# Performance work log

Hardware: AMD Instinct MI355X
Metric: run time of the kernel (lower is better)

The kernel has to match this reference:

```python
import jax, jax.numpy as jnp
import numpy as np


def setup_inputs() -> dict:
    key = jax.random.key(0)
    k1, k2, k3, k4 = jax.random.split(key, 4)
    B, C, N, T = 16, 64, 2048, 24
    x = jax.random.normal(k1, (B, C, N, T), dtype=jnp.float32)
    adj = jax.random.uniform(k2, (N, N), dtype=jnp.float32)
    # Learned parameters (initialized to zeros in the original; random here
    # so the reference exercises nontrivial math).
    Gw = jax.random.normal(k3, (T, T), dtype=jnp.float32) * 0.1
    alpha = jax.random.normal(k4, (C,), dtype=jnp.float32) * 0.1
    return {"x": x, "adj": adj, "Gw": Gw, "alpha": alpha}


def reference(x, adj, Gw, alpha):
    # k = q = einsum('bcnt,c->bnt')  (channel-reduced features)
    k = jnp.einsum('bcnt,c->bnt', x, alpha)
    # scores[b,n,m] = k[b,n,:] @ Gw @ k[b,m,:]
    kG = jnp.einsum('bnt,ts->bns', k, Gw)          # [B,N,T]
    scores = jnp.einsum('bns,bms->bnm', kG, k)     # [B,N,N]
    att = jax.nn.softmax(scores, axis=-1)
    # adjacency-masked weighted aggregation over neighbors
    return jnp.einsum('bnm,bcmt->bcnt', att * adj, x)
```

## Files before the change

### kernel.cpp

```cpp
#include <hip/hip_runtime.h>
#include <hip/hip_bf16.h>

#define BB 16
#define CC 64
#define NN 2048
#define TT 24
#define JJ (CC*TT)
#define NT (NN*TT)

typedef unsigned short u16;
typedef unsigned int u32;
typedef __bf16 bf16x8 __attribute__((ext_vector_type(8)));
typedef u16 u16x8 __attribute__((ext_vector_type(8)));
typedef float f32x4 __attribute__((ext_vector_type(4)));
typedef u32 u32x4 __attribute__((ext_vector_type(4)));

static __device__ __forceinline__ u16 f2bf(float f) {
  union { float f; u32 u; } v; v.f = f;
  u32 u = v.u;
  u += 0x7fffu + ((u >> 16) & 1u);
  return (u16)(u >> 16);
}
static __device__ __forceinline__ float bf2f(u16 h) {
  union { u32 u; float f; } v; v.u = ((u32)h) << 16; return v.f;
}
static __device__ __forceinline__ bf16x8 ld_bf8(const u16* p) {
  return __builtin_bit_cast(bf16x8, *(const u16x8*)p);
}
#define MFMA16(a,b,c) __builtin_amdgcn_mfma_f32_16x16x32_bf16((a),(b),(c),0,0,0)

static __device__ __forceinline__ void gload16(const u16* g, u16* lds) {
  __builtin_amdgcn_global_load_lds(
      (const __attribute__((address_space(1))) u32*)g,
      (__attribute__((address_space(3))) u32*)lds, 16, 0, 0);
}

__global__ __launch_bounds__(256) void kA(
    const float* __restrict__ x, const float* __restrict__ alpha,
    u16* __restrict__ xT, float* __restrict__ kpart) {
  int bid = blockIdx.x;
  int b  = bid >> 5;
  int mt = (bid >> 1) & 15;
  int ch = bid & 1;
  int m0 = mt * 128;
  int tid = threadIdx.x;
  __shared__ float tile[128][25];
  float kacc[12];
  #pragma unroll
  for (int e = 0; e < 12; ++e) kacc[e] = 0.f;

  for (int c = ch*32; c < ch*32 + 32; ++c) {
    const float4* src4 = (const float4*)(x + ((size_t)(b*CC + c)*NN + m0)*TT);
    float a = alpha[c];
    float4 v[3];
    #pragma unroll
    for (int q = 0; q < 3; ++q) v[q] = src4[tid*3 + q];
    __syncthreads();
    #pragma unroll
    for (int q = 0; q < 3; ++q) {
      int idx = tid*3 + q;
      int mm = idx / 6, off = (idx - mm*6)*4;
      tile[mm][off]   = v[q].x; tile[mm][off+1] = v[q].y;
      tile[mm][off+2] = v[q].z; tile[mm][off+3] = v[q].w;
      kacc[q*4+0] += a*v[q].x; kacc[q*4+1] += a*v[q].y;
      kacc[q*4+2] += a*v[q].z; kacc[q*4+3] += a*v[q].w;
    }
    __syncthreads();
    #pragma unroll
    for (int qq = 0; qq < 6; ++qq) {
      int idx = tid*6 + qq;
      int t = idx >> 6, mp = idx & 63;
      u32 lo = f2bf(tile[2*mp][t]);
      u32 hi = f2bf(tile[2*mp+1][t]);
      ((u32*)(xT + ((size_t)((b*CC + c)*TT + t))*NN + m0))[mp] = lo | (hi << 16);
    }
  }
  float* kp = kpart + (size_t)ch*BB*NT + (size_t)b*NT + (size_t)m0*TT + tid*12;
  #pragma unroll
  for (int q = 0; q < 3; ++q)
    *(float4*)(kp + q*4) = make_float4(kacc[q*4], kacc[q*4+1], kacc[q*4+2], kacc[q*4+3]);
}

__global__ __launch_bounds__(256) void k2_prep(
    const float* __restrict__ kpart, const float* __restrict__ Gw,
    u16* __restrict__ kGhi, u16* __restrict__ kGlo,
    u16* __restrict__ kPhi, u16* __restrict__ kPlo) {
  __shared__ float gw[TT*TT];
  for (int i = threadIdx.x; i < TT*TT; i += 256) gw[i] = Gw[i];
  __syncthreads();
  int row = blockIdx.x * blockDim.x + threadIdx.x;
  if (row >= BB*NN) return;
  float kr[TT];
  const float4* s0 = (const float4*)(kpart + (size_t)row*TT);
  const float4* s1 = (const float4*)(kpart + (size_t)BB*NT + (size_t)row*TT);
  #pragma unroll
  for (int q = 0; q < 6; ++q) {
    float4 a = s0[q], bv = s1[q];
    kr[4*q]   = a.x + bv.x; kr[4*q+1] = a.y + bv.y;
    kr[4*q+2] = a.z + bv.z; kr[4*q+3] = a.w + bv.w;
  }
  float o[TT];
  #pragma unroll
  for (int s = 0; s < TT; ++s) o[s] = 0.f;
  #pragma unroll
  for (int t = 0; t < TT; ++t) {
    float kv = kr[t];
    #pragma unroll
    for (int s = 0; s < TT; ++s) o[s] += kv * gw[t*TT + s];
  }
  size_t rb = (size_t)row * 32;
  u32* ghi = (u32*)(kGhi + rb); u32* glo = (u32*)(kGlo + rb);
  u32* phi = (u32*)(kPhi + rb); u32* plo = (u32*)(kPlo + rb);
  #pragma unroll
  for (int sp = 0; sp < 16; ++sp) {
    float v0 = (2*sp   < TT) ? o[2*sp]   : 0.f;
    float v1 = (2*sp+1 < TT) ? o[2*sp+1] : 0.f;
    u16 h0 = f2bf(v0), h1 = f2bf(v1);
    u16 l0 = f2bf(v0 - bf2f(h0)), l1 = f2bf(v1 - bf2f(h1));
    ghi[sp] = (u32)h0 | ((u32)h1 << 16);
    glo[sp] = (u32)l0 | ((u32)l1 << 16);
    float w0 = (2*sp   < TT) ? kr[2*sp]   : 0.f;
    float w1 = (2*sp+1 < TT) ? kr[2*sp+1] : 0.f;
    u16 ph0 = f2bf(w0), ph1 = f2bf(w1);
    u16 pl0 = f2bf(w0 - bf2f(ph0)), pl1 = f2bf(w1 - bf2f(ph1));
    phi[sp] = (u32)ph0 | ((u32)ph1 << 16);
    plo[sp] = (u32)pl0 | ((u32)pl1 << 16);
  }
}

__global__ __launch_bounds__(256) void kW(
    const u16* __restrict__ kGhi, const u16* __restrict__ kGlo,
    const u16* __restrict__ kPhi, const u16* __restrict__ kPlo,
    const float* __restrict__ adj, u16* __restrict__ Wm,
    float* __restrict__ Zpart) {
  int bid = blockIdx.x;
  int b = bid >> 8, nt = (bid >> 4) & 15, mt = bid & 15;
  int tid = threadIdx.x;
  int w = tid >> 6, l = tid & 63;
  __shared__ u16 wlds[128][128];
  size_t kgb = ((size_t)b*NN + nt*128) * 32;
  bf16x8 ahi[2], alo[2];
  #pragma unroll
  for (int nf = 0; nf < 2; ++nf) {
    size_t off = kgb + (size_t)(w*32 + nf*16 + (l & 15))*32 + (l >> 4)*8;
    ahi[nf] = ld_bf8(kGhi + off);
    alo[nf] = ld_bf8(kGlo + off);
  }
  f32x4 acc[2][8];
  #pragma unroll
  for (int mf = 0; mf < 8; ++mf) {
    size_t off = ((size_t)b*NN + mt*128 + mf*16 + (l & 15))*32 + (l >> 4)*8;
    bf16x8 bhi = ld_bf8(kPhi + off);
    bf16x8 blo = ld_bf8(kPlo + off);
    #pragma unroll
    for (int nf = 0; nf < 2; ++nf) {
      f32x4 a = {0.f, 0.f, 0.f, 0.f};
      a = MFMA16(ahi[nf], blo, a);
      a = MFMA16(alo[nf], bhi, a);
      a = MFMA16(ahi[nf], bhi, a);
      acc[nf][mf] = a;
    }
  }
  #pragma unroll
  for (int nf = 0; nf < 2; ++nf)
    #pragma unroll
    for (int r = 0; r < 4; ++r) {
      int nl = w*32 + nf*16 + (l >> 4)*4 + r;
      float rs = 0.f;
      #pragma unroll
      for (int mf = 0; mf < 8; ++mf) {
        int ml = mf*16 + (l & 15);
        float e = __expf(acc[nf][mf][r]);
        rs += e;
        float wv = e * adj[(size_t)(nt*128 + nl)*NN + mt*128 + ml];
        wlds[nl][ml] = f2bf(wv);
      }
      #pragma unroll
      for (int st = 1; st < 16; st <<= 1) rs += __shfl_xor(rs, st);
      if ((l & 15) == 0)
        Zpart[((size_t)b*NN + nt*128 + nl)*16 + mt] = rs;
    }
  __syncthreads();
  int row = tid >> 1, half = tid & 1;
  const u32x4* s4 = (const u32x4*)&wlds[row][half*64];
  u32x4* d4 = (u32x4*)(Wm + ((size_t)(b*NN + nt*128 + row))*NN + mt*128 + half*64);
  #pragma unroll
  for (int q = 0; q < 8; ++q) d4[q] = s4[q];
}

__global__ __launch_bounds__(256) void kZ(
    const float* __restrict__ Zpart, float* __restrict__ rinvg) {
  int i = blockIdx.x * 256 + threadIdx.x;
  const float4* zp = (const float4*)(Zpart + (size_t)i*16);
  float4 a = zp[0], b = zp[1], c = zp[2], d = zp[3];
  float s = a.x+a.y+a.z+a.w + b.x+b.y+b.z+b.w
          + c.x+c.y+c.z+c.w + d.x+d.y+d.z+d.w;
  rinvg[i] = 1.f / s;
}

__global__ __launch_bounds__(512, 2) void k4_gemm(
    const u16* __restrict__ Wm, const u16* __restrict__ xT,
    const float* __restrict__ rinvg, float* __restrict__ out) {
  __shared__ __align__(16) u16 sA[2*2*128*64];
  __shared__ __align__(16) u16 sB[2*2*128*64];
  __shared__ float rinv[256];

  int bid = blockIdx.x;
  int wg = (bid & 7) * 96 + (bid >> 3);
  int b = wg / 48; int rem = wg - b*48;
  int nt = rem / 6, jt = rem - nt*6;

  int tid = threadIdx.x;
  int w = tid >> 6, l = tid & 63;
  int wr = w >> 2, wc = w & 3;
  int l15 = l & 15, l4 = l >> 4, lx = l & 7;

  int g0 = ((l4)     ^ lx) << 3;
  int g1 = ((4 + l4) ^ lx) << 3;
  int rbA = wr*8192 + l15*64;
  int rbB = (wc>>1)*8192 + ((wc&1)*64 + l15)*64;

  int srow = tid >> 3, sslot = tid & 7;
  int sgx = (sslot ^ (srow & 7)) << 3;
  const size_t ROW64 = (size_t)64 * NN;
  const u16* pAlo = Wm + (size_t)b*NN*NN + (size_t)(nt*256 + srow)*NN + sgx;
  const u16* pAhi = pAlo + (size_t)128*NN;
  const u16* pBlo = xT + (size_t)b*JJ*NN + (size_t)(jt*256 + srow)*NN + sgx;
  const u16* pBhi = pBlo + (size_t)128*NN;
  int wbase = w << 9;

#define STG(ptr, arr, dbuf, half) do { \
    gload16(ptr, arr + ((dbuf)<<14) + ((half)<<13) + wbase); \
    gload16(ptr + ROW64, arr + ((dbuf)<<14) + ((half)<<13) + 4096 + wbase); \
    ptr += 64; } while (0)

  f32x4 acc[8][4];
  #pragma unroll
  for (int f = 0; f < 8; ++f)
    #pragma unroll
    for (int cf = 0; cf < 4; ++cf) acc[f][cf] = (f32x4){0.f,0.f,0.f,0.f};
  bf16x8 a[4][2], bv[4][2];

  if (tid < 256) rinv[tid] = rinvg[(size_t)b*NN + nt*256 + tid];
  __builtin_amdgcn_sched_barrier(0);
  STG(pBlo, sB, 0, 0); STG(pBhi, sB, 0, 1);
  STG(pAlo, sA, 0, 0); STG(pAhi, sA, 0, 1);
  STG(pBlo, sB, 1, 0); STG(pBhi, sB, 1, 1);
  STG(pAlo, sA, 1, 0);
  asm volatile("s_waitcnt vmcnt(6)" ::: "memory");
  __builtin_amdgcn_sched_barrier(0);
  __builtin_amdgcn_s_barrier();

  for (int kt = 0; kt < 32; ++kt) {
    int p = kt & 1, q = p ^ 1;
    int pb = p << 14;
    #pragma unroll
    for (int f = 0; f < 4; ++f) {
      a[f][0] = ld_bf8(sA + pb + rbA + f*1024 + g0);
      a[f][1] = ld_bf8(sA + pb + rbA + f*1024 + g1);
    }
    #pragma unroll
    for (int cf = 0; cf < 2; ++cf) {
      bv[cf][0] = ld_bf8(sB + pb + rbB + cf*1024 + g0);
      bv[cf][1] = ld_bf8(sB + pb + rbB + cf*1024 + g1);
    }
    if (kt < 31) STG(pAhi, sA, q, 1);
    __builtin_amdgcn_s_barrier();
    asm volatile("s_waitcnt lgkmcnt(0)" ::: "memory");
    __builtin_amdgcn_sched_barrier(0);
    __builtin_amdgcn_s_setprio(1);
    #pragma unroll
    for (int f = 0; f < 4; ++f)
      #pragma unroll
      for (int cf = 0; cf < 2; ++cf) {
        acc[f][cf] = MFMA16(a[f][0], bv[cf][0], acc[f][cf]);
        acc[f][cf] = MFMA16(a[f][1], bv[cf][1], acc[f][cf]);
      }
    __builtin_amdgcn_s_setprio(0);
    __builtin_amdgcn_s_barrier();
    #pragma unroll
    for (int cf = 2; cf < 4; ++cf) {
      bv[cf][0] = ld_bf8(sB + pb + rbB + cf*1024 + g0);
      bv[cf][1] = ld_bf8(sB + pb + rbB + cf*1024 + g1);
    }
    __builtin_amdgcn_s_barrier();
    asm volatile("s_waitcnt lgkmcnt(0)" ::: "memory");
    __builtin_amdgcn_sched_barrier(0);
    __builtin_amdgcn_s_setprio(1);
    #pragma unroll
    for (int f = 0; f < 4; ++f)
      #pragma unroll
      for (int cf = 2; cf < 4; ++cf) {
        acc[f][cf] = MFMA16(a[f][0], bv[cf][0], acc[f][cf]);
        acc[f][cf] = MFMA16(a[f][1], bv[cf][1], acc[f][cf]);
      }
    __builtin_amdgcn_s_setprio(0);
    __builtin_amdgcn_s_barrier();
    #pragma unroll
    for (int f = 0; f < 4; ++f) {
      a[f][0] = ld_bf8(sA + pb + rbA + (f+4)*1024 + g0);
      a[f][1] = ld_bf8(sA + pb + rbA + (f+4)*1024 + g1);
    }
    if (kt < 30) STG(pBlo, sB, p, 0);
    __builtin_amdgcn_s_barrier();
    asm volatile("s_waitcnt lgkmcnt(0)" ::: "memory");
    __builtin_amdgcn_sched_barrier(0);
    __builtin_amdgcn_s_setprio(1);
    #pragma unroll
    for (int f = 0; f < 4; ++f)
      #pragma unroll
      for (int cf = 0; cf < 2; ++cf) {
        acc[f+4][cf] = MFMA16(a[f][0], bv[cf][0], acc[f+4][cf]);
        acc[f+4][cf] = MFMA16(a[f][1], bv[cf][1], acc[f+4][cf]);
      }
    __builtin_amdgcn_s_setprio(0);
    __builtin_amdgcn_s_barrier();
    if (kt < 30) { STG(pBhi, sB, p, 1); STG(pAlo, sA, p, 0); }
    __builtin_amdgcn_s_barrier();
    __builtin_amdgcn_s_setprio(1);
    #pragma unroll
    for (int f = 0; f < 4; ++f)
      #pragma unroll
      for (int cf = 2; cf < 4; ++cf) {
        acc[f+4][cf] = MFMA16(a[f][0], bv[cf][0], acc[f+4][cf]);
        acc[f+4][cf] = MFMA16(a[f][1], bv[cf][1], acc[f+4][cf]);
      }
    __builtin_amdgcn_s_setprio(0);
    if (kt < 30) {
      asm volatile("s_waitcnt vmcnt(6)" ::: "memory");
      __builtin_amdgcn_sched_barrier(0);
      __builtin_amdgcn_s_barrier();
    } else if (kt == 30) {
      asm volatile("s_waitcnt vmcnt(0)" ::: "memory");
      __builtin_amdgcn_sched_barrier(0);
      __builtin_amdgcn_s_barrier();
    }
  }
#undef STG

  #pragma unroll
  for (int f = 0; f < 8; ++f)
    #pragma unroll
    for (int cf = 0; cf < 4; ++cf) {
      int j = jt*256 + wc*64 + cf*16 + l15;
      int c = j / TT, t_ = j - c*TT;
      #pragma unroll
      for (int r = 0; r < 4; ++r) {
        int nl = wr*128 + f*16 + l4*4 + r;
        out[((size_t)(b*CC + c)*NN + nt*256 + nl)*TT + t_] = acc[f][cf][r] * rinv[nl];
      }
    }
}

extern "C" void kernel_launch(void* const* d_in, const int* in_sizes, int n_in,
                              void* d_out, int out_size, void* d_ws, size_t ws_size,
                              hipStream_t stream) {
  const float* x     = (const float*)d_in[0];
  const float* adj   = (const float*)d_in[1];
  const float* Gw    = (const float*)d_in[2];
  const float* alpha = (const float*)d_in[3];
  float* out = (float*)d_out;

  const size_t XT_B = (size_t)BB*JJ*NN*2;
  const size_t W_B  = (size_t)BB*NN*NN*2;
  const size_t KS_B = (size_t)BB*NN*32*2;
  const size_t ZP_B = (size_t)BB*NN*16*4;
  char* base = (char*)d_ws;
  u16*   xT    = (u16*)base;
  u16*   Wm    = (u16*)(base + XT_B);
  float* kpart = (float*)(base + XT_B);
  u16*   kGhi  = (u16*)(base + XT_B + W_B);
  u16*   kGlo  = (u16*)(base + XT_B + W_B + KS_B);
  u16*   kPhi  = (u16*)(base + XT_B + W_B + 2*KS_B);
  u16*   kPlo  = (u16*)(base + XT_B + W_B + 3*KS_B);
  float* Zpart = (float*)(base + XT_B + W_B + 4*KS_B);
  float* rinvg = (float*)(base + XT_B + W_B + 4*KS_B + ZP_B);

  kA<<<512, 256, 0, stream>>>(x, alpha, xT, kpart);
  k2_prep<<<BB*NN/256, 256, 0, stream>>>(kpart, Gw, kGhi, kGlo, kPhi, kPlo);
  kW<<<BB*16*16, 256, 0, stream>>>(kGhi, kGlo, kPhi, kPlo, adj, Wm, Zpart);
  kZ<<<BB*NN/256, 256, 0, stream>>>(Zpart, rinvg);
  k4_gemm<<<768, 512, 0, stream>>>(Wm, xT, rinvg, out);
}
```

Measured before the change: 426.0 us.

## Replace fine-grained 8-phase GEMM pipeline with simple double-buffered K-loop

Rewrites the main k4_gemm K-loop. The old interleaved schedule had many barriers and half-tile staging; the new one prefetches the whole next 256x64 A/B tile into the alternate LDS buffer, waits once per iteration, and issues all 32 MFMAs per k-half with split lgkmcnt waits. This cuts barrier count and scheduling complexity, at the cost of less fine-grained overlap between global loads and MFMA. The epilogue now reads rinv straight from global memory instead of LDS and hoists the column index divisions out of the store loop.

```diff
diff --git a/kernel.cpp b/kernel.cpp
--- a/kernel.cpp
+++ b/kernel.cpp
@@ -201,9 +201,8 @@
 __global__ __launch_bounds__(512, 2) void k4_gemm(
     const u16* __restrict__ Wm, const u16* __restrict__ xT,
     const float* __restrict__ rinvg, float* __restrict__ out) {
-  __shared__ __align__(16) u16 sA[2*2*128*64];
-  __shared__ __align__(16) u16 sB[2*2*128*64];
-  __shared__ float rinv[256];
+  __shared__ __align__(16) u16 sA[2*256*64];
+  __shared__ __align__(16) u16 sB[2*256*64];
 
   int bid = blockIdx.x;
   int wg = (bid & 7) * 96 + (bid >> 3);
@@ -218,137 +217,93 @@
   int g0 = ((l4)     ^ lx) << 3;
   int g1 = ((4 + l4) ^ lx) << 3;
   int rbA = wr*8192 + l15*64;
-  int rbB = (wc>>1)*8192 + ((wc&1)*64 + l15)*64;
+  int rbB = wc*4096 + l15*64;
 
   int srow = tid >> 3, sslot = tid & 7;
   int sgx = (sslot ^ (srow & 7)) << 3;
   const size_t ROW64 = (size_t)64 * NN;
-  const u16* pAlo = Wm + (size_t)b*NN*NN + (size_t)(nt*256 + srow)*NN + sgx;
-  const u16* pAhi = pAlo + (size_t)128*NN;
-  const u16* pBlo = xT + (size_t)b*JJ*NN + (size_t)(jt*256 + srow)*NN + sgx;
-  const u16* pBhi = pBlo + (size_t)128*NN;
+  const u16* pA = Wm + (size_t)b*NN*NN + (size_t)(nt*256 + srow)*NN + sgx;
+  const u16* pB = xT + (size_t)b*JJ*NN + (size_t)(jt*256 + srow)*NN + sgx;
   int wbase = w << 9;
 
-#define STG(ptr, arr, dbuf, half) do { \
-    gload16(ptr, arr + ((dbuf)<<14) + ((half)<<13) + wbase); \
-    gload16(ptr + ROW64, arr + ((dbuf)<<14) + ((half)<<13) + 4096 + wbase); \
-    ptr += 64; } while (0)
-
   f32x4 acc[8][4];
   #pragma unroll
   for (int f = 0; f < 8; ++f)
     #pragma unroll
     for (int cf = 0; cf < 4; ++cf) acc[f][cf] = (f32x4){0.f,0.f,0.f,0.f};
-  bf16x8 a[4][2], bv[4][2];
-
-  if (tid < 256) rinv[tid] = rinvg[(size_t)b*NN + nt*256 + tid];
-  __builtin_amdgcn_sched_barrier(0);
-  STG(pBlo, sB, 0, 0); STG(pBhi, sB, 0, 1);
-  STG(pAlo, sA, 0, 0); STG(pAhi, sA, 0, 1);
-  STG(pBlo, sB, 1, 0); STG(pBhi, sB, 1, 1);
-  STG(pAlo, sA, 1, 0);
-  asm volatile("s_waitcnt vmcnt(6)" ::: "memory");
-  __builtin_amdgcn_sched_barrier(0);
-  __builtin_amdgcn_s_barrier();
+
+  #pragma unroll
+  for (int i = 0; i < 4; ++i) gload16(pA + (size_t)i*ROW64, sA + i*4096 + wbase);
+  #pragma unroll
+  for (int i = 0; i < 4; ++i) gload16(pB + (size_t)i*ROW64, sB + i*4096 + wbase);
+  pA += 64; pB += 64;
 
   for (int kt = 0; kt < 32; ++kt) {
-    int p = kt & 1, q = p ^ 1;
-    int pb = p << 14;
-    #pragma unroll
-    for (int f = 0; f < 4; ++f) {
-      a[f][0] = ld_bf8(sA + pb + rbA + f*1024 + g0);
-      a[f][1] = ld_bf8(sA + pb + rbA + f*1024 + g1);
-    }
-    #pragma unroll
-    for (int cf = 0; cf < 2; ++cf) {
-      bv[cf][0] = ld_bf8(sB + pb + rbB + cf*1024 + g0);
-      bv[cf][1] = ld_bf8(sB + pb + rbB + cf*1024 + g1);
-    }
-    if (kt < 31) STG(pAhi, sA, q, 1);
+    int pb = (kt & 1) << 14;
+    int qb = pb ^ 16384;
+    if (kt < 31) {
+      #pragma unroll
+      for (int i = 0; i < 4; ++i) gload16(pA + (size_t)i*ROW64, sA + qb + i*4096 + wbase);
+      #pragma unroll
+      for (int i = 0; i < 4; ++i) gload16(pB + (size_t)i*ROW64, sB + qb + i*4096 + wbase);
+      pA += 64; pB += 64;
+      asm volatile("s_waitcnt vmcnt(8)" ::: "memory");
+    } else {
+      asm volatile("s_waitcnt vmcnt(0)" ::: "memory");
+    }
+    __builtin_amdgcn_sched_barrier(0);
     __builtin_amdgcn_s_barrier();
+    __builtin_amdgcn_sched_barrier(0);
+
+    bf16x8 a0[8], b0[4], a1[8], b1[4];
+    #pragma unroll
+    for (int f = 0; f < 8; ++f) a0[f] = ld_bf8(sA + pb + rbA + f*1024 + g0);
+    #pragma unroll
+    for (int cf = 0; cf < 4; ++cf) b0[cf] = ld_bf8(sB + pb + rbB + cf*1024 + g0);
+    __builtin_amdgcn_sched_barrier(0);
+    #pragma unroll
+    for (int f = 0; f < 8; ++f) a1[f] = ld_bf8(sA + pb + rbA + f*1024 + g1);
+    #pragma unroll
+    for (int cf = 0; cf < 4; ++cf) b1[cf] = ld_bf8(sB + pb + rbB + cf*1024 + g1);
+
+    asm volatile("s_waitcnt lgkmcnt(12)" ::: "memory");
+    __builtin_amdgcn_sched_barrier(0);
+    __builtin_amdgcn_s_setprio(1);
+    #pragma unroll
+    for (int f = 0; f < 8; ++f)
+      #pragma unroll
+      for (int cf = 0; cf < 4; ++cf)
+        acc[f][cf] = MFMA16(a0[f], b0[cf], acc[f][cf]);
+    __builtin_amdgcn_s_setprio(0);
+
     asm volatile("s_waitcnt lgkmcnt(0)" ::: "memory");
     __builtin_amdgcn_sched_barrier(0);
     __builtin_amdgcn_s_setprio(1);
     #pragma unroll
-    for (int f = 0; f < 4; ++f)
-      #pragma unroll
-      for (int cf = 0; cf < 2; ++cf) {
-        acc[f][cf] = MFMA16(a[f][0], bv[cf][0], acc[f][cf]);
-        acc[f][cf] = MFMA16(a[f][1], bv[cf][1], acc[f][cf]);
-      }
+    for (int f = 0; f < 8; ++f)
+      #pragma unroll
+      for (int cf = 0; cf < 4; ++cf)
+        acc[f][cf] = MFMA16(a1[f], b1[cf], acc[f][cf]);
     __builtin_amdgcn_s_setprio(0);
     __builtin_amdgcn_s_barrier();
-    #pragma unroll
-    for (int cf = 2; cf < 4; ++cf) {
-      bv[cf][0] = ld_bf8(sB + pb + rbB + cf*1024 + g0);
-      bv[cf][1] = ld_bf8(sB + pb + rbB + cf*1024 + g1);
-    }
-    __builtin_amdgcn_s_barrier();
-    asm volatile("s_waitcnt lgkmcnt(0)" ::: "memory");
-    __builtin_amdgcn_sched_barrier(0);
-    __builtin_amdgcn_s_setprio(1);
-    #pragma unroll
-    for (int f = 0; f < 4; ++f)
-      #pragma unroll
-      for (int cf = 2; cf < 4; ++cf) {
-        acc[f][cf] = MFMA16(a[f][0], bv[cf][0], acc[f][cf]);
-        acc[f][cf] = MFMA16(a[f][1], bv[cf][1], acc[f][cf]);
-      }
-    __builtin_amdgcn_s_setprio(0);
-    __builtin_amdgcn_s_barrier();
-    #pragma unroll
-    for (int f = 0; f < 4; ++f) {
-      a[f][0] = ld_bf8(sA + pb + rbA + (f+4)*1024 + g0);
-      a[f][1] = ld_bf8(sA + pb + rbA + (f+4)*1024 + g1);
-    }
-    if (kt < 30) STG(pBlo, sB, p, 0);
-    __builtin_amdgcn_s_barrier();
-    asm volatile("s_waitcnt lgkmcnt(0)" ::: "memory");
-    __builtin_amdgcn_sched_barrier(0);
-    __builtin_amdgcn_s_setprio(1);
-    #pragma unroll
-    for (int f = 0; f < 4; ++f)
-      #pragma unroll
-      for (int cf = 0; cf < 2; ++cf) {
-        acc[f+4][cf] = MFMA16(a[f][0], bv[cf][0], acc[f+4][cf]);
-        acc[f+4][cf] = MFMA16(a[f][1], bv[cf][1], acc[f+4][cf]);
-      }
-    __builtin_amdgcn_s_setprio(0);
-    __builtin_amdgcn_s_barrier();
-    if (kt < 30) { STG(pBhi, sB, p, 1); STG(pAlo, sA, p, 0); }
-    __builtin_amdgcn_s_barrier();
-    __builtin_amdgcn_s_setprio(1);
-    #pragma unroll
-    for (int f = 0; f < 4; ++f)
-      #pragma unroll
-      for (int cf = 2; cf < 4; ++cf) {
-        acc[f+4][cf] = MFMA16(a[f][0], bv[cf][0], acc[f+4][cf]);
-        acc[f+4][cf] = MFMA16(a[f][1], bv[cf][1], acc[f+4][cf]);
-      }
-    __builtin_amdgcn_s_setprio(0);
-    if (kt < 30) {
-      asm volatile("s_waitcnt vmcnt(6)" ::: "memory");
-      __builtin_amdgcn_sched_barrier(0);
-      __builtin_amdgcn_s_barrier();
-    } else if (kt == 30) {
-      asm volatile("s_waitcnt vmcnt(0)" ::: "memory");
-      __builtin_amdgcn_sched_barrier(0);
-      __builtin_amdgcn_s_barrier();
-    }
-  }
-#undef STG
-
+  }
+
+  const float* rb_ = rinvg + (size_t)b*NN + nt*256 + wr*128;
+  int cj[4], tj4[4];
+  #pragma unroll
+  for (int cf = 0; cf < 4; ++cf) {
+    int j = jt*256 + wc*64 + cf*16 + l15;
+    cj[cf] = j / TT; tj4[cf] = j - cj[cf]*TT;
+  }
   #pragma unroll
   for (int f = 0; f < 8; ++f)
     #pragma unroll
-    for (int cf = 0; cf < 4; ++cf) {
-      int j = jt*256 + wc*64 + cf*16 + l15;
-      int c = j / TT, t_ = j - c*TT;
-      #pragma unroll
-      for (int r = 0; r < 4; ++r) {
-        int nl = wr*128 + f*16 + l4*4 + r;
-        out[((size_t)(b*CC + c)*NN + nt*256 + nl)*TT + t_] = acc[f][cf][r] * rinv[nl];
-      }
+    for (int r = 0; r < 4; ++r) {
+      int nl = wr*128 + f*16 + l4*4 + r;
+      float rv = rb_[f*16 + l4*4 + r];
+      #pragma unroll
+      for (int cf = 0; cf < 4; ++cf)
+        out[((size_t)(b*CC + cj[cf])*NN + nt*256 + nl)*TT + tj4[cf]] = acc[f][cf][r] * rv;
     }
 }
 
```

Result: no change. 420.3 us (-1.4%).
